# Optimization experiments

Measured on AMD Instinct MI355X. Metric: run time of the kernel, lower is better.

Reference implementation:

```python
import jax, jax.numpy as jnp
from jax import lax
import numpy as np

CASCADES = 3
CH = 16  # hidden channels of BasicBlock denoiser

# ---- finite-difference operators (equivalent to the sparse matrices) ----
# D has rows i<n-1: (-1 at i, +1 at i+1); last row zero.  (D v)[i] = v[i+1]-v[i], last = 0.

def fdiff(v, axis):
    d = jnp.diff(v, axis=axis)
    pad = [(0, 0)] * v.ndim
    pad[axis] = (0, 1)
    return jnp.pad(d, pad)

# Exact transpose: (D^T u)[j] = u[j-1] - u[j], with u[-1]=0 and the -u term dropped at j=n-1.

def fdiff_t(u, axis):
    n = u.shape[axis]
    pad_f = [(0, 0)] * u.ndim
    pad_f[axis] = (1, 0)
    u_prev = lax.slice_in_dim(jnp.pad(u, pad_f), 0, n, axis=axis)
    pad_b = [(0, 0)] * u.ndim
    pad_b[axis] = (0, 1)
    u_m = jnp.pad(lax.slice_in_dim(u, 0, n - 1, axis=axis), pad_b)
    return u_prev - u_m

# ---- BasicBlock: residual 3-layer 3D CNN denoiser ----

def _conv3d(h, w, b):
    out = lax.conv_general_dilated(h, w, (1, 1, 1), 'SAME',
                                   dimension_numbers=('NCDHW', 'OIDHW', 'NCDHW'))
    return out + b[None, :, None, None, None]

def basic_block(x, w1, b1, w2, b2, w3, b3):
    # x: [B, D, H, W]
    h = x[:, None]  # [B,1,D,H,W]
    h = jax.nn.relu(_conv3d(h, w1, b1))
    h = jax.nn.relu(_conv3d(h, w2, b2))
    h = _conv3d(h, w3, b3)
    return x + h[:, 0]

# ---- BeijingGeometry surrogate: parallel-beam fidelity A^T(sino - A t), A = sum over depth ----

def ite(t, sino):
    depth = t.shape[1]
    res = sino - t.sum(axis=1)          # [B, H, W]
    return jnp.broadcast_to(res[:, None] / depth, t.shape)


def setup_inputs() -> dict:
    key = jax.random.key(0)
    ks = jax.random.split(key, 12)
    B, D, H, W = 1, 64, 128, 128
    return {
        'image': jax.random.normal(ks[0], (B, D, H, W), jnp.float32),
        'sino': jax.random.normal(ks[1], (B, H, W), jnp.float32),
        'ae_w1': 0.05 * jax.random.normal(ks[2], (4, CH, 1, 3, 3, 3), jnp.float32),
        'ae_b1': jnp.zeros((4, CH), jnp.float32),
        'ae_w2': 0.05 * jax.random.normal(ks[3], (4, CH, CH, 3, 3, 3), jnp.float32),
        'ae_b2': jnp.zeros((4, CH), jnp.float32),
        'ae_w3': 0.05 * jax.random.normal(ks[4], (4, 1, CH, 3, 3, 3), jnp.float32),
        'ae_b3': jnp.zeros((4, 1), jnp.float32),
        'ntx': 0.1 * jax.random.normal(ks[5], (CASCADES,), jnp.float32),
        'nty': 0.1 * jax.random.normal(ks[6], (CASCADES,), jnp.float32),
        'ntz': 0.1 * jax.random.normal(ks[7], (CASCADES,), jnp.float32),
        'nt': 0.1 * jax.random.normal(ks[8], (CASCADES,), jnp.float32),
    }


def reference(image, sino, ae_w1, ae_b1, ae_w2, ae_b2, ae_w3, ae_b3, ntx, nty, ntz, nt):
    # axes: 1 = z (depth), 2 = y, 3 = x
    ae = lambda i, x: basic_block(x, ae_w1[i], ae_b1[i], ae_w2[i], ae_b2[i], ae_w3[i], ae_b3[i])
    t = image
    p = q = s = jnp.zeros_like(image)
    outs = [image]
    for c in range(CASCADES):
        z = t + ite(t, sino)
        pnew = ae(0, fdiff(z, 3))
        qnew = ae(1, fdiff(z, 2))
        snew = ae(2, fdiff(z, 1))
        znew = ae(3, z)
        p = p + ntx[c] * (p - pnew)
        q = q + nty[c] * (q - qnew)
        s = s + ntz[c] * (s - snew)
        z_ = t + nt[c] * (t - znew)
        t = fdiff_t(p, 3) + fdiff_t(q, 2) + fdiff_t(s, 1) + z_
        outs.append(t)
    return jnp.stack(outs)  # [cascades+1, B, D, H, W]
```

## Files before the change

### kernel.cpp

```cpp
#include <hip/hip_runtime.h>
#include <cstddef>

#define DD 64
#define HH 128
#define WW 128
#define HWC (HH * WW)
#define NN (DD * HWC)

#define PD 66
#define PH 130
#define PW 130
#define PHW (PH * PW)
#define PN (PD * PHW)

typedef __attribute__((ext_vector_type(8))) _Float16 half8;
typedef __attribute__((ext_vector_type(2))) _Float16 h2;
typedef __attribute__((ext_vector_type(4))) float f32x4;
typedef __attribute__((ext_vector_type(2))) float f32x2;

__device__ __forceinline__ int pcidx(int d, int h, int w) {
    return (d + 1) * PHW + (h + 1) * PW + (w + 1);
}

__device__ __forceinline__ float fdot2f(h2 a, h2 b, float c) {
#if __has_builtin(__builtin_amdgcn_fdot2)
    return __builtin_amdgcn_fdot2(a, b, c, false);
#else
    return fmaf((float)a[0], (float)b[0], fmaf((float)a[1], (float)b[1], c));
#endif
}

__global__ __launch_bounds__(256) void pad_zero(float* __restrict__ zP,
                                                float* __restrict__ dxP,
                                                float* __restrict__ dyP,
                                                float* __restrict__ dzP,
                                                _Float16* __restrict__ h1,
                                                _Float16* __restrict__ h2b) {
    int idx = blockIdx.x * 256 + threadIdx.x;
    if (idx >= PN) return;
    int d = idx / PHW;
    int rem = idx - d * PHW;
    int h = rem / PW;
    int w = rem - h * PW;
    bool pad = (d == 0) | (d == PD - 1) | (h == 0) | (h == PH - 1) |
               (w == 0) | (w == PW - 1);
    if (!pad) return;
    zP[idx] = 0.f;
    dxP[idx] = 0.f;
    dyP[idx] = 0.f;
    dzP[idx] = 0.f;
    half8 z = {};
    *(half8*)(h1 + (size_t)idx * 16) = z;
    *(half8*)(h1 + (size_t)idx * 16 + 8) = z;
    *(half8*)(h2b + (size_t)idx * 16) = z;
    *(half8*)(h2b + (size_t)idx * 16 + 8) = z;
}

__global__ __launch_bounds__(256) void init_k(const float* __restrict__ img,
                                              float* __restrict__ t,
                                              float* __restrict__ out0,
                                              float* __restrict__ p,
                                              float* __restrict__ q,
                                              float* __restrict__ s) {
    int i = blockIdx.x * 256 + threadIdx.x;
    float v = img[i];
    t[i] = v;
    out0[i] = v;
    p[i] = 0.f;
    q[i] = 0.f;
    s[i] = 0.f;
}

__global__ __launch_bounds__(256) void colsum_k(const float* __restrict__ t,
                                                const float* __restrict__ sino,
                                                float* __restrict__ r) {
    int hw = blockIdx.x * 256 + threadIdx.x;
    float sum = 0.f;
#pragma unroll 8
    for (int d = 0; d < DD; ++d) sum += t[d * HWC + hw];
    r[hw] = (sino[hw] - sum) * (1.0f / DD);
}

__global__ __launch_bounds__(256) void zdiff_k(const float* __restrict__ t,
                                               const float* __restrict__ r,
                                               float* __restrict__ zP,
                                               float* __restrict__ dxP,
                                               float* __restrict__ dyP,
                                               float* __restrict__ dzP) {
    int i = blockIdx.x * 256 + threadIdx.x;
    int w = i & (WW - 1);
    int h = (i >> 7) & (HH - 1);
    int d = i >> 14;
    int hw = i & (HWC - 1);
    int pc = pcidx(d, h, w);
    float tv = t[i];
    float rv = r[hw];
    float zv = tv + rv;
    zP[pc] = zv;
    dxP[pc] = (w < WW - 1) ? (t[i + 1] + r[hw + 1]) - zv : 0.f;
    dyP[pc] = (h < HH - 1) ? (t[i + WW] + r[hw + WW]) - zv : 0.f;
    dzP[pc] = (d < DD - 1) ? (t[i + HWC] - tv) : 0.f;
}

__global__ __launch_bounds__(256) void prep_w1(const float* __restrict__ w1,
                                               float* __restrict__ wA) {
    int idx = blockIdx.x * 256 + threadIdx.x;
    if (idx >= 1728) return;
    int bi = idx / 432;
    int rem = idx - bi * 432;
    int tap = rem >> 4;
    int co = rem & 15;
    wA[idx] = w1[bi * 432 + co * 27 + tap];
}

__global__ __launch_bounds__(256) void prep_w2(const float* __restrict__ w2,
                                               _Float16* __restrict__ wB) {
    int idx = blockIdx.x * 256 + threadIdx.x;
    if (idx >= 3584) return;
    int bi = idx / 896;
    int rem = idx - bi * 896;
    int kc = rem >> 4;
    int co = rem & 15;
    int tap = kc >> 1;
    int ci0 = (kc & 1) * 8;
    half8 v;
#pragma unroll
    for (int j = 0; j < 8; ++j) {
        float f = (tap < 27) ? w2[bi * 6912 + (co * 16 + ci0 + j) * 27 + tap] : 0.f;
        v[j] = (_Float16)f;
    }
    *(half8*)(wB + (size_t)idx * 8) = v;
}

__global__ __launch_bounds__(256) void prep_w3(const float* __restrict__ w3,
                                               h2* __restrict__ wC) {
    int idx = blockIdx.x * 256 + threadIdx.x;
    if (idx >= 864) return;
    int bi = idx / 216;
    int rem = idx - bi * 216;
    int tap = rem >> 3;
    int j = rem & 7;
    h2 v;
    v[0] = (_Float16)w3[bi * 432 + (2 * j) * 27 + tap];
    v[1] = (_Float16)w3[bi * 432 + (2 * j + 1) * 27 + tap];
    wC[idx] = v;
}

__global__ __launch_bounds__(256) void conv1_k(const float* __restrict__ x,
                                               const float* __restrict__ wA,
                                               const float* __restrict__ bias,
                                               _Float16* __restrict__ out) {
    int i = blockIdx.x * 256 + threadIdx.x;
    int w0 = (i & 31) * 4;
    int h = (i >> 5) & (HH - 1);
    int d = i >> 12;
    int pc = pcidx(d, h, w0);

    float acc[4][16];
#pragma unroll
    for (int o = 0; o < 4; ++o)
#pragma unroll
        for (int co = 0; co < 16; ++co) acc[o][co] = bias[co];

#pragma unroll
    for (int kd = 0; kd < 3; ++kd)
#pragma unroll
        for (int kh = 0; kh < 3; ++kh) {
            const float* base = x + pc + (kd - 1) * PHW + (kh - 1) * PW;
            f32x4 u = *(const f32x4*)(base - 1);
            f32x2 v = *(const f32x2*)(base + 3);
            float c[6] = {u[0], u[1], u[2], u[3], v[0], v[1]};
#pragma unroll
            for (int kw = 0; kw < 3; ++kw) {
                const int tap = (kd * 3 + kh) * 3 + kw;
                const float* wt = wA + tap * 16;
#pragma unroll
                for (int o = 0; o < 4; ++o) {
                    float vv = c[o + kw];
#pragma unroll
                    for (int co = 0; co < 16; ++co)
                        acc[o][co] = fmaf(vv, wt[co], acc[o][co]);
                }
            }
        }

#pragma unroll
    for (int o = 0; o < 4; ++o) {
        half8 lo, hi;
#pragma unroll
        for (int co = 0; co < 8; ++co) {
            lo[co] = (_Float16)fmaxf(acc[o][co], 0.f);
            hi[co] = (_Float16)fmaxf(acc[o][co + 8], 0.f);
        }
        _Float16* po = out + (size_t)(pc + o) * 16;
        *(half8*)po = lo;
        *(half8*)(po + 8) = hi;
    }
}

__global__ __launch_bounds__(256) void conv2_mfma(const _Float16* __restrict__ x,
                                                  const _Float16* __restrict__ wB,
                                                  const float* __restrict__ bias,
                                                  _Float16* __restrict__ out) {
    const int tid = threadIdx.x;
    const int lane = tid & 63;
    const int wid = tid >> 6;
    const int m64 = blockIdx.x * 256 + wid * 64;
    const int w0 = m64 & (WW - 1);
    const int h0 = (m64 >> 7) & (HH - 1);
    const int d0 = m64 >> 14;
    const int pc64 = pcidx(d0, h0, w0);
    const int l15 = lane & 15;
    const int lg = lane >> 4;
    const int tapSel = lg >> 1;
    const int ci0 = (lg & 1) * 8;

    int offl[14];
#pragma unroll
    for (int t = 0; t < 14; ++t) {
        int tap = 2 * t + tapSel;
        if (tap > 26) tap = 26;
        int kd = tap / 9;
        int kh = (tap / 3) % 3;
        int kw = tap % 3;
        offl[t] = (kd - 1) * PHW + (kh - 1) * PW + (kw - 1);
    }

    f32x4 acc0 = {0.f, 0.f, 0.f, 0.f};
    f32x4 acc1 = acc0, acc2 = acc0, acc3 = acc0;
    const int arow = pc64 + l15;

#pragma unroll
    for (int t = 0; t < 14; ++t) {
        half8 b = *(const half8*)(wB + (size_t)((t * 4 + lg) * 16 + l15) * 8);
        int ab = (arow + offl[t]) * 16 + ci0;
        half8 a0 = *(const half8*)(x + ab);
        half8 a1 = *(const half8*)(x + ab + 16 * 16);
        half8 a2 = *(const half8*)(x + ab + 32 * 16);
        half8 a3 = *(const half8*)(x + ab + 48 * 16);
        acc0 = __builtin_amdgcn_mfma_f32_16x16x32_f16(a0, b, acc0, 0, 0, 0);
        acc1 = __builtin_amdgcn_mfma_f32_16x16x32_f16(a1, b, acc1, 0, 0, 0);
        acc2 = __builtin_amdgcn_mfma_f32_16x16x32_f16(a2, b, acc2, 0, 0, 0);
        acc3 = __builtin_amdgcn_mfma_f32_16x16x32_f16(a3, b, acc3, 0, 0, 0);
    }

    float bc = bias[l15];
#pragma unroll
    for (int r = 0; r < 4; ++r) {
        f32x4 a = (r == 0) ? acc0 : (r == 1) ? acc1 : (r == 2) ? acc2 : acc3;
#pragma unroll
        for (int reg = 0; reg < 4; ++reg) {
            int prow = pc64 + r * 16 + lg * 4 + reg;
            float v = fmaxf(a[reg] + bc, 0.f);
            out[(size_t)prow * 16 + l15] = (_Float16)v;
        }
    }
}

__global__ __launch_bounds__(256) void conv3_k(const _Float16* __restrict__ x,
                                               const h2* __restrict__ wC,
                                               const float* __restrict__ bias,
                                               const float* __restrict__ residP,
                                               float* __restrict__ out) {
    int i = blockIdx.x * 256 + threadIdx.x;
    int w = i & (WW - 1);
    int h = (i >> 7) & (HH - 1);
    int dq = i >> 14;
    int d0 = dq * 4;
    int pc = pcidx(d0, h, w);

    float accA[4] = {0.f, 0.f, 0.f, 0.f};
    float accB[4] = {0.f, 0.f, 0.f, 0.f};

#pragma unroll
    for (int kh = 0; kh < 3; ++kh)
#pragma unroll
        for (int kw = 0; kw < 3; ++kw) {
            const _Float16* base =
                x + (size_t)(pc - PHW + (kh - 1) * PW + (kw - 1)) * 16;
#pragma unroll
            for (int p = 0; p < 6; ++p) {
                const _Float16* px = base + (size_t)p * PHW * 16;
                half8 v0 = *(const half8*)px;
                half8 v1 = *(const half8*)(px + 8);
#pragma unroll
                for (int kd = 0; kd < 3; ++kd) {
                    const int o = p - kd;
                    if (o < 0 || o > 3) continue;
                    const h2* wv = wC + (size_t)(kd * 9 + kh * 3 + kw) * 8;
                    h2 t2;
                    float a = accA[o], b = accB[o];
                    t2[0] = v0[0]; t2[1] = v0[1]; a = fdot2f(t2, wv[0], a);
                    t2[0] = v0[2]; t2[1] = v0[3]; b = fdot2f(t2, wv[1], b);
                    t2[0] = v0[4]; t2[1] = v0[5]; a = fdot2f(t2, wv[2], a);
                    t2[0] = v0[6]; t2[1] = v0[7]; b = fdot2f(t2, wv[3], b);
                    t2[0] = v1[0]; t2[1] = v1[1]; a = fdot2f(t2, wv[4], a);
                    t2[0] = v1[2]; t2[1] = v1[3]; b = fdot2f(t2, wv[5], b);
                    t2[0] = v1[4]; t2[1] = v1[5]; a = fdot2f(t2, wv[6], a);
                    t2[0] = v1[6]; t2[1] = v1[7]; b = fdot2f(t2, wv[7], b);
                    accA[o] = a; accB[o] = b;
                }
            }
        }

    float bc = bias[0];
    int ob = (d0 << 14) + (h << 7) + w;
#pragma unroll
    for (int o = 0; o < 4; ++o)
        out[ob + o * HWC] = residP[pc + o * PHW] + bc + (accA[o] + accB[o]);
}

__global__ __launch_bounds__(256) void update_k(const float* __restrict__ p0,
                                                const float* __restrict__ q0,
                                                const float* __restrict__ s0,
                                                const float* __restrict__ pn,
                                                const float* __restrict__ qn,
                                                const float* __restrict__ sn,
                                                const float* __restrict__ zn,
                                                float* __restrict__ t,
                                                float* __restrict__ p1,
                                                float* __restrict__ q1,
                                                float* __restrict__ s1,
                                                float* __restrict__ out,
                                                const float* __restrict__ ntx,
                                                const float* __restrict__ nty,
                                                const float* __restrict__ ntz,
                                                const float* __restrict__ nt,
                                                int c) {
    int i = blockIdx.x * 256 + threadIdx.x;
    int w = i & (WW - 1);
    int h = (i >> 7) & (HH - 1);
    int d = i >> 14;
    float cx = ntx[c], cy = nty[c], cz = ntz[c], ct = nt[c];

    float pu = p0[i] + cx * (p0[i] - pn[i]);
    float qu = q0[i] + cy * (q0[i] - qn[i]);
    float su = s0[i] + cz * (s0[i] - sn[i]);
    p1[i] = pu;
    q1[i] = qu;
    s1[i] = su;

    float tv = t[i];
    float zl = tv + ct * (tv - zn[i]);

    float acc = zl;
    if (w > 0) {
        float a = p0[i - 1];
        acc += a + cx * (a - pn[i - 1]);
    }
    if (w < WW - 1) acc -= pu;
    if (h > 0) {
        float a = q0[i - WW];
        acc += a + cy * (a - qn[i - WW]);
    }
    if (h < HH - 1) acc -= qu;
    if (d > 0) {
        float a = s0[i - HWC];
        acc += a + cz * (a - sn[i - HWC]);
    }
    if (d < DD - 1) acc -= su;

    t[i] = acc;
    out[i] = acc;
}

extern "C" void kernel_launch(void* const* d_in, const int* in_sizes, int n_in,
                              void* d_out, int out_size, void* d_ws, size_t ws_size,
                              hipStream_t stream) {
    const float* image = (const float*)d_in[0];
    const float* sino  = (const float*)d_in[1];
    const float* w1    = (const float*)d_in[2];
    const float* b1    = (const float*)d_in[3];
    const float* w2    = (const float*)d_in[4];
    const float* b2    = (const float*)d_in[5];
    const float* w3    = (const float*)d_in[6];
    const float* b3    = (const float*)d_in[7];
    const float* ntx   = (const float*)d_in[8];
    const float* nty   = (const float*)d_in[9];
    const float* ntz   = (const float*)d_in[10];
    const float* nt    = (const float*)d_in[11];

    float* out = (float*)d_out;
    float* ws  = (float*)d_ws;

    float* t     = ws;
    float* pbuf[2] = {ws + (size_t)1 * NN, ws + (size_t)4 * NN};
    float* qbuf[2] = {ws + (size_t)2 * NN, ws + (size_t)5 * NN};
    float* sbuf[2] = {ws + (size_t)3 * NN, ws + (size_t)6 * NN};
    float* pn = ws + (size_t)7 * NN;
    float* qn = ws + (size_t)8 * NN;
    float* sn = ws + (size_t)9 * NN;
    float* zn = ws + (size_t)10 * NN;
    float* r  = ws + (size_t)11 * NN;

    float* padbase = ws + (size_t)12 * NN;
    float* zP  = padbase;
    float* dxP = padbase + (size_t)1 * PN;
    float* dyP = padbase + (size_t)2 * PN;
    float* dzP = padbase + (size_t)3 * PN;
    _Float16* h1 = (_Float16*)(padbase + (size_t)4 * PN);
    _Float16* h2b = (_Float16*)(padbase + (size_t)12 * PN);
    _Float16* wBp = (_Float16*)(padbase + (size_t)20 * PN);
    h2* wCp = (h2*)(wBp + 4 * 7168);
    float* wAp = padbase + (size_t)20 * PN + 16384;

    const int NB = NN / 256;
    const int HB = HWC / 256;
    const int QB = NN / 4 / 256;
    const int PB = (PN + 255) / 256;

    pad_zero<<<PB, 256, 0, stream>>>(zP, dxP, dyP, dzP, h1, h2b);
    prep_w1<<<7, 256, 0, stream>>>(w1, wAp);
    prep_w2<<<14, 256, 0, stream>>>(w2, wBp);
    prep_w3<<<4, 256, 0, stream>>>(w3, wCp);
    init_k<<<NB, 256, 0, stream>>>(image, t, out, pbuf[0], qbuf[0], sbuf[0]);

    int cur = 0;
    for (int c = 0; c < 3; ++c) {
        colsum_k<<<HB, 256, 0, stream>>>(t, sino, r);
        zdiff_k<<<NB, 256, 0, stream>>>(t, r, zP, dxP, dyP, dzP);

        const float* xinP[4] = {dxP, dyP, dzP, zP};
        float*       oae[4]  = {pn, qn, sn, zn};
        for (int bi = 0; bi < 4; ++bi) {
            conv1_k<<<QB, 256, 0, stream>>>(xinP[bi], wAp + (size_t)bi * 432,
                                            b1 + (size_t)bi * 16, h1);
            conv2_mfma<<<NB, 256, 0, stream>>>(h1, wBp + (size_t)bi * 7168,
                                               b2 + (size_t)bi * 16, h2b);
            conv3_k<<<QB, 256, 0, stream>>>(h2b, wCp + (size_t)bi * 216,
                                            b3 + (size_t)bi, xinP[bi], oae[bi]);
        }

        update_k<<<NB, 256, 0, stream>>>(pbuf[cur], qbuf[cur], sbuf[cur],
                                         pn, qn, sn, zn, t,
                                         pbuf[1 - cur], qbuf[1 - cur], sbuf[1 - cur],
                                         out + (size_t)(c + 1) * NN,
                                         ntx, nty, ntz, nt, c);
        cur ^= 1;
    }
}
```

Measured before the change: 1.229 ms.

## Batch the four denoiser branches into single grid launches per conv stage

The four BasicBlock branches each ran their own conv1/conv2/conv3 launches. They now run as one launch per conv stage, using blockIdx.y to pick the branch, with a separate fp16 intermediate buffer per branch when the workspace is large enough. The three weight-prep kernels are also merged into one launch. This cuts the kernel launch count and the serialization between small grids, and fills the GPU better. In exchange it needs about four times the intermediate buffer memory and keeps a fallback path that loops over branches.

```diff
diff --git a/kernel.cpp b/kernel.cpp
--- a/kernel.cpp
+++ b/kernel.cpp
@@ -34,8 +34,9 @@
                                                 float* __restrict__ dxP,
                                                 float* __restrict__ dyP,
                                                 float* __restrict__ dzP,
-                                                _Float16* __restrict__ h1,
-                                                _Float16* __restrict__ h2b) {
+                                                _Float16* __restrict__ h1all,
+                                                _Float16* __restrict__ h2all,
+                                                int nb, size_t hstride) {
     int idx = blockIdx.x * 256 + threadIdx.x;
     if (idx >= PN) return;
     int d = idx / PHW;
@@ -50,10 +51,14 @@
     dyP[idx] = 0.f;
     dzP[idx] = 0.f;
     half8 z = {};
-    *(half8*)(h1 + (size_t)idx * 16) = z;
-    *(half8*)(h1 + (size_t)idx * 16 + 8) = z;
-    *(half8*)(h2b + (size_t)idx * 16) = z;
-    *(half8*)(h2b + (size_t)idx * 16 + 8) = z;
+    for (int k = 0; k < nb; ++k) {
+        _Float16* p1 = h1all + (size_t)k * hstride + (size_t)idx * 16;
+        _Float16* p2 = h2all + (size_t)k * hstride + (size_t)idx * 16;
+        *(half8*)p1 = z;
+        *(half8*)(p1 + 8) = z;
+        *(half8*)p2 = z;
+        *(half8*)(p2 + 8) = z;
+    }
 }
 
 __global__ __launch_bounds__(256) void init_k(const float* __restrict__ img,
@@ -102,54 +107,59 @@
     dzP[pc] = (d < DD - 1) ? (t[i + HWC] - tv) : 0.f;
 }
 
-__global__ __launch_bounds__(256) void prep_w1(const float* __restrict__ w1,
-                                               float* __restrict__ wA) {
+__global__ __launch_bounds__(256) void prep_all(const float* __restrict__ w1,
+                                                const float* __restrict__ w2,
+                                                const float* __restrict__ w3,
+                                                float* __restrict__ wA,
+                                                _Float16* __restrict__ wB,
+                                                h2* __restrict__ wC) {
     int idx = blockIdx.x * 256 + threadIdx.x;
-    if (idx >= 1728) return;
-    int bi = idx / 432;
-    int rem = idx - bi * 432;
-    int tap = rem >> 4;
-    int co = rem & 15;
-    wA[idx] = w1[bi * 432 + co * 27 + tap];
-}
-
-__global__ __launch_bounds__(256) void prep_w2(const float* __restrict__ w2,
-                                               _Float16* __restrict__ wB) {
-    int idx = blockIdx.x * 256 + threadIdx.x;
-    if (idx >= 3584) return;
-    int bi = idx / 896;
-    int rem = idx - bi * 896;
-    int kc = rem >> 4;
-    int co = rem & 15;
-    int tap = kc >> 1;
-    int ci0 = (kc & 1) * 8;
-    half8 v;
-#pragma unroll
-    for (int j = 0; j < 8; ++j) {
-        float f = (tap < 27) ? w2[bi * 6912 + (co * 16 + ci0 + j) * 27 + tap] : 0.f;
-        v[j] = (_Float16)f;
-    }
-    *(half8*)(wB + (size_t)idx * 8) = v;
-}
-
-__global__ __launch_bounds__(256) void prep_w3(const float* __restrict__ w3,
-                                               h2* __restrict__ wC) {
-    int idx = blockIdx.x * 256 + threadIdx.x;
-    if (idx >= 864) return;
-    int bi = idx / 216;
-    int rem = idx - bi * 216;
-    int tap = rem >> 3;
-    int j = rem & 7;
-    h2 v;
-    v[0] = (_Float16)w3[bi * 432 + (2 * j) * 27 + tap];
-    v[1] = (_Float16)w3[bi * 432 + (2 * j + 1) * 27 + tap];
-    wC[idx] = v;
-}
-
-__global__ __launch_bounds__(256) void conv1_k(const float* __restrict__ x,
+    if (idx < 1728) {
+        int bi = idx / 432;
+        int rem = idx - bi * 432;
+        int tap = rem >> 4;
+        int co = rem & 15;
+        wA[idx] = w1[bi * 432 + co * 27 + tap];
+    } else if (idx < 5312) {
+        int k = idx - 1728;
+        int bi = k / 896;
+        int rem = k - bi * 896;
+        int kc = rem >> 4;
+        int co = rem & 15;
+        int tap = kc >> 1;
+        int ci0 = (kc & 1) * 8;
+        half8 v;
+#pragma unroll
+        for (int j = 0; j < 8; ++j) {
+            float f = (tap < 27) ? w2[bi * 6912 + (co * 16 + ci0 + j) * 27 + tap]
+                                 : 0.f;
+            v[j] = (_Float16)f;
+        }
+        *(half8*)(wB + (size_t)k * 8) = v;
+    } else if (idx < 6176) {
+        int k = idx - 5312;
+        int bi = k / 216;
+        int rem = k - bi * 216;
+        int tap = rem >> 3;
+        int j = rem & 7;
+        h2 v;
+        v[0] = (_Float16)w3[bi * 432 + (2 * j) * 27 + tap];
+        v[1] = (_Float16)w3[bi * 432 + (2 * j + 1) * 27 + tap];
+        wC[k] = v;
+    }
+}
+
+__global__ __launch_bounds__(256) void conv1_b(const float* __restrict__ padbase,
                                                const float* __restrict__ wA,
-                                               const float* __restrict__ bias,
-                                               _Float16* __restrict__ out) {
+                                               const float* __restrict__ b1,
+                                               _Float16* __restrict__ h1all,
+                                               size_t hstride, int bi_base) {
+    const int bi = bi_base + blockIdx.y;
+    const float* x = padbase + (size_t)PN * ((bi + 1) & 3);
+    const float* wAb = wA + bi * 432;
+    const float* bias = b1 + bi * 16;
+    _Float16* out = h1all + (size_t)bi * hstride;
+
     int i = blockIdx.x * 256 + threadIdx.x;
     int w0 = (i & 31) * 4;
     int h = (i >> 5) & (HH - 1);
@@ -173,7 +183,7 @@
 #pragma unroll
             for (int kw = 0; kw < 3; ++kw) {
                 const int tap = (kd * 3 + kh) * 3 + kw;
-                const float* wt = wA + tap * 16;
+                const float* wt = wAb + tap * 16;
 #pragma unroll
                 for (int o = 0; o < 4; ++o) {
                     float vv = c[o + kw];
@@ -198,10 +208,17 @@
     }
 }
 
-__global__ __launch_bounds__(256) void conv2_mfma(const _Float16* __restrict__ x,
-                                                  const _Float16* __restrict__ wB,
-                                                  const float* __restrict__ bias,
-                                                  _Float16* __restrict__ out) {
+__global__ __launch_bounds__(256) void conv2_b(const _Float16* __restrict__ h1all,
+                                               const _Float16* __restrict__ wB,
+                                               const float* __restrict__ b2,
+                                               _Float16* __restrict__ h2all,
+                                               size_t hstride, int bi_base) {
+    const int bi = bi_base + blockIdx.y;
+    const _Float16* x = h1all + (size_t)bi * hstride;
+    const _Float16* wBb = wB + (size_t)bi * 7168;
+    const float* bias = b2 + bi * 16;
+    _Float16* out = h2all + (size_t)bi * hstride;
+
     const int tid = threadIdx.x;
     const int lane = tid & 63;
     const int wid = tid >> 6;
@@ -232,7 +249,7 @@
 
 #pragma unroll
     for (int t = 0; t < 14; ++t) {
-        half8 b = *(const half8*)(wB + (size_t)((t * 4 + lg) * 16 + l15) * 8);
+        half8 b = *(const half8*)(wBb + (size_t)((t * 4 + lg) * 16 + l15) * 8);
         int ab = (arow + offl[t]) * 16 + ci0;
         half8 a0 = *(const half8*)(x + ab);
         half8 a1 = *(const half8*)(x + ab + 16 * 16);
@@ -257,11 +274,19 @@
     }
 }
 
-__global__ __launch_bounds__(256) void conv3_k(const _Float16* __restrict__ x,
+__global__ __launch_bounds__(256) void conv3_b(const _Float16* __restrict__ h2all,
                                                const h2* __restrict__ wC,
-                                               const float* __restrict__ bias,
-                                               const float* __restrict__ residP,
-                                               float* __restrict__ out) {
+                                               const float* __restrict__ b3,
+                                               const float* __restrict__ padbase,
+                                               float* __restrict__ pnBase,
+                                               size_t hstride, int bi_base) {
+    const int bi = bi_base + blockIdx.y;
+    const _Float16* x = h2all + (size_t)bi * hstride;
+    const h2* wCb = wC + (size_t)bi * 216;
+    const float* residP = padbase + (size_t)PN * ((bi + 1) & 3);
+    float* out = pnBase + (size_t)bi * NN;
+    const float bc = b3[bi];
+
     int i = blockIdx.x * 256 + threadIdx.x;
     int w = i & (WW - 1);
     int h = (i >> 7) & (HH - 1);
@@ -287,7 +312,7 @@
                 for (int kd = 0; kd < 3; ++kd) {
                     const int o = p - kd;
                     if (o < 0 || o > 3) continue;
-                    const h2* wv = wC + (size_t)(kd * 9 + kh * 3 + kw) * 8;
+                    const h2* wv = wCb + (size_t)(kd * 9 + kh * 3 + kw) * 8;
                     h2 t2;
                     float a = accA[o], b = accB[o];
                     t2[0] = v0[0]; t2[1] = v0[1]; a = fdot2f(t2, wv[0], a);
@@ -303,7 +328,6 @@
             }
         }
 
-    float bc = bias[0];
     int ob = (d0 << 14) + (h << 7) + w;
 #pragma unroll
     for (int o = 0; o < 4; ++o)
@@ -388,9 +412,6 @@
     float* qbuf[2] = {ws + (size_t)2 * NN, ws + (size_t)5 * NN};
     float* sbuf[2] = {ws + (size_t)3 * NN, ws + (size_t)6 * NN};
     float* pn = ws + (size_t)7 * NN;
-    float* qn = ws + (size_t)8 * NN;
-    float* sn = ws + (size_t)9 * NN;
-    float* zn = ws + (size_t)10 * NN;
     float* r  = ws + (size_t)11 * NN;
 
     float* padbase = ws + (size_t)12 * NN;
@@ -398,21 +419,28 @@
     float* dxP = padbase + (size_t)1 * PN;
     float* dyP = padbase + (size_t)2 * PN;
     float* dzP = padbase + (size_t)3 * PN;
-    _Float16* h1 = (_Float16*)(padbase + (size_t)4 * PN);
-    _Float16* h2b = (_Float16*)(padbase + (size_t)12 * PN);
-    _Float16* wBp = (_Float16*)(padbase + (size_t)20 * PN);
+
+    const size_t HS = (size_t)PN * 16;
+    _Float16* h1all = (_Float16*)(padbase + (size_t)4 * PN);
+    size_t needed_batched =
+        ((size_t)12 * NN + (size_t)4 * PN + 17000) * 4 + 2 * 4 * HS * 2;
+    bool batched = ws_size >= needed_batched;
+    int nb = batched ? 4 : 1;
+    size_t hstride = batched ? HS : 0;
+
+    _Float16* h2all = h1all + (size_t)nb * HS;
+    float* wtail = (float*)(h2all + (size_t)nb * HS);
+    _Float16* wBp = (_Float16*)wtail;
     h2* wCp = (h2*)(wBp + 4 * 7168);
-    float* wAp = padbase + (size_t)20 * PN + 16384;
+    float* wAp = (float*)(wCp + 4 * 216);
 
     const int NB = NN / 256;
     const int HB = HWC / 256;
     const int QB = NN / 4 / 256;
     const int PB = (PN + 255) / 256;
 
-    pad_zero<<<PB, 256, 0, stream>>>(zP, dxP, dyP, dzP, h1, h2b);
-    prep_w1<<<7, 256, 0, stream>>>(w1, wAp);
-    prep_w2<<<14, 256, 0, stream>>>(w2, wBp);
-    prep_w3<<<4, 256, 0, stream>>>(w3, wCp);
+    pad_zero<<<PB, 256, 0, stream>>>(zP, dxP, dyP, dzP, h1all, h2all, nb, HS);
+    prep_all<<<25, 256, 0, stream>>>(w1, w2, w3, wAp, wBp, wCp);
     init_k<<<NB, 256, 0, stream>>>(image, t, out, pbuf[0], qbuf[0], sbuf[0]);
 
     int cur = 0;
@@ -420,19 +448,27 @@
         colsum_k<<<HB, 256, 0, stream>>>(t, sino, r);
         zdiff_k<<<NB, 256, 0, stream>>>(t, r, zP, dxP, dyP, dzP);
 
-        const float* xinP[4] = {dxP, dyP, dzP, zP};
-        float*       oae[4]  = {pn, qn, sn, zn};
-        for (int bi = 0; bi < 4; ++bi) {
-            conv1_k<<<QB, 256, 0, stream>>>(xinP[bi], wAp + (size_t)bi * 432,
-                                            b1 + (size_t)bi * 16, h1);
-            conv2_mfma<<<NB, 256, 0, stream>>>(h1, wBp + (size_t)bi * 7168,
-                                               b2 + (size_t)bi * 16, h2b);
-            conv3_k<<<QB, 256, 0, stream>>>(h2b, wCp + (size_t)bi * 216,
-                                            b3 + (size_t)bi, xinP[bi], oae[bi]);
+        if (batched) {
+            conv1_b<<<dim3(QB, 4), 256, 0, stream>>>(padbase, wAp, b1, h1all,
+                                                     hstride, 0);
+            conv2_b<<<dim3(NB, 4), 256, 0, stream>>>(h1all, wBp, b2, h2all,
+                                                     hstride, 0);
+            conv3_b<<<dim3(QB, 4), 256, 0, stream>>>(h2all, wCp, b3, padbase,
+                                                     pn, hstride, 0);
+        } else {
+            for (int bi = 0; bi < 4; ++bi) {
+                conv1_b<<<dim3(QB, 1), 256, 0, stream>>>(padbase, wAp, b1,
+                                                         h1all, 0, bi);
+                conv2_b<<<dim3(NB, 1), 256, 0, stream>>>(h1all, wBp, b2,
+                                                         h2all, 0, bi);
+                conv3_b<<<dim3(QB, 1), 256, 0, stream>>>(h2all, wCp, b3,
+                                                         padbase, pn, 0, bi);
+            }
         }
 
         update_k<<<NB, 256, 0, stream>>>(pbuf[cur], qbuf[cur], sbuf[cur],
-                                         pn, qn, sn, zn, t,
+                                         pn, pn + NN, pn + 2 * (size_t)NN,
+                                         pn + 3 * (size_t)NN, t,
                                          pbuf[1 - cur], qbuf[1 - cur], sbuf[1 - cur],
                                          out + (size_t)(c + 1) * NN,
                                          ntx, nty, ntz, nt, c);
```

New measurement: 1.223 ms. About the same (-0.4%).

## Stage conv2 input halo tile in LDS via direct global-to-LDS loads

Applied to the files above, without the earlier changes.

The middle 16->16 channel convolution now stages the padded input tile, 2 rows by 4 planes in the halo region with 130-wide rows, into shared memory using global_load_lds. A swizzled half-row layout is used to reduce bank conflicts. MFMA A-operands are then read from LDS instead of issuing 27-tap redundant global loads, which cuts L2/global traffic. Each block now covers two h-rows of 128 instead of four 64-voxel strips. The three weight-prep kernels are merged into one launch, and the buffer layout is compacted. The LDS footprint of about 53KB per block may reduce occupancy.

```diff
diff --git a/kernel.cpp b/kernel.cpp
--- a/kernel.cpp
+++ b/kernel.cpp
@@ -102,48 +102,46 @@
     dzP[pc] = (d < DD - 1) ? (t[i + HWC] - tv) : 0.f;
 }
 
-__global__ __launch_bounds__(256) void prep_w1(const float* __restrict__ w1,
-                                               float* __restrict__ wA) {
+__global__ __launch_bounds__(256) void prep_all(const float* __restrict__ w1,
+                                                const float* __restrict__ w2,
+                                                const float* __restrict__ w3,
+                                                float* __restrict__ wA,
+                                                _Float16* __restrict__ wB,
+                                                h2* __restrict__ wC) {
     int idx = blockIdx.x * 256 + threadIdx.x;
-    if (idx >= 1728) return;
-    int bi = idx / 432;
-    int rem = idx - bi * 432;
-    int tap = rem >> 4;
-    int co = rem & 15;
-    wA[idx] = w1[bi * 432 + co * 27 + tap];
-}
-
-__global__ __launch_bounds__(256) void prep_w2(const float* __restrict__ w2,
-                                               _Float16* __restrict__ wB) {
-    int idx = blockIdx.x * 256 + threadIdx.x;
-    if (idx >= 3584) return;
-    int bi = idx / 896;
-    int rem = idx - bi * 896;
-    int kc = rem >> 4;
-    int co = rem & 15;
-    int tap = kc >> 1;
-    int ci0 = (kc & 1) * 8;
-    half8 v;
-#pragma unroll
-    for (int j = 0; j < 8; ++j) {
-        float f = (tap < 27) ? w2[bi * 6912 + (co * 16 + ci0 + j) * 27 + tap] : 0.f;
-        v[j] = (_Float16)f;
-    }
-    *(half8*)(wB + (size_t)idx * 8) = v;
-}
-
-__global__ __launch_bounds__(256) void prep_w3(const float* __restrict__ w3,
-                                               h2* __restrict__ wC) {
-    int idx = blockIdx.x * 256 + threadIdx.x;
-    if (idx >= 864) return;
-    int bi = idx / 216;
-    int rem = idx - bi * 216;
-    int tap = rem >> 3;
-    int j = rem & 7;
-    h2 v;
-    v[0] = (_Float16)w3[bi * 432 + (2 * j) * 27 + tap];
-    v[1] = (_Float16)w3[bi * 432 + (2 * j + 1) * 27 + tap];
-    wC[idx] = v;
+    if (idx < 1728) {
+        int bi = idx / 432;
+        int rem = idx - bi * 432;
+        int tap = rem >> 4;
+        int co = rem & 15;
+        wA[idx] = w1[bi * 432 + co * 27 + tap];
+    } else if (idx < 5312) {
+        int k = idx - 1728;
+        int bi = k / 896;
+        int rem = k - bi * 896;
+        int kc = rem >> 4;
+        int co = rem & 15;
+        int tap = kc >> 1;
+        int ci0 = (kc & 1) * 8;
+        half8 v;
+#pragma unroll
+        for (int j = 0; j < 8; ++j) {
+            float f = (tap < 27) ? w2[bi * 6912 + (co * 16 + ci0 + j) * 27 + tap]
+                                 : 0.f;
+            v[j] = (_Float16)f;
+        }
+        *(half8*)(wB + (size_t)k * 8) = v;
+    } else if (idx < 6176) {
+        int k = idx - 5312;
+        int bi = k / 216;
+        int rem = k - bi * 216;
+        int tap = rem >> 3;
+        int j = rem & 7;
+        h2 v;
+        v[0] = (_Float16)w3[bi * 432 + (2 * j) * 27 + tap];
+        v[1] = (_Float16)w3[bi * 432 + (2 * j + 1) * 27 + tap];
+        wC[k] = v;
+    }
 }
 
 __global__ __launch_bounds__(256) void conv1_k(const float* __restrict__ x,
@@ -198,24 +196,43 @@
     }
 }
 
-__global__ __launch_bounds__(256) void conv2_mfma(const _Float16* __restrict__ x,
-                                                  const _Float16* __restrict__ wB,
-                                                  const float* __restrict__ bias,
-                                                  _Float16* __restrict__ out) {
+__global__ __launch_bounds__(256) void conv2_lds(const _Float16* __restrict__ x,
+                                                 const _Float16* __restrict__ wB,
+                                                 const float* __restrict__ bias,
+                                                 _Float16* __restrict__ out) {
+    __shared__ __align__(16) _Float16 lds[3328 * 8];
+
     const int tid = threadIdx.x;
     const int lane = tid & 63;
     const int wid = tid >> 6;
-    const int m64 = blockIdx.x * 256 + wid * 64;
-    const int w0 = m64 & (WW - 1);
-    const int h0 = (m64 >> 7) & (HH - 1);
-    const int d0 = m64 >> 14;
-    const int pc64 = pcidx(d0, h0, w0);
+    const int m256 = blockIdx.x * 256;
+    const int h0 = (m256 >> 7) & (HH - 1);
+    const int d0 = m256 >> 14;
+    const int origin = d0 * PHW + h0 * PW;
+
+    for (int it = 0; it < 13; ++it) {
+        int P = it * 256 + tid;
+        int G = P ^ ((P >> 3) & 1);
+        int lin = G >> 1;
+        int hf = G & 1;
+        unsigned seg = (unsigned)lin / 130u;
+        int wx = lin - (int)seg * 130;
+        int dz = (int)seg >> 2, hy = (int)seg & 3;
+        const _Float16* src =
+            x + ((size_t)(origin + dz * PHW + hy * PW + wx) * 16 + hf * 8);
+        _Float16* dst = lds + ((size_t)(it * 256 + wid * 64) * 8);
+        __builtin_amdgcn_global_load_lds(
+            (const __attribute__((address_space(1))) void*)src,
+            (__attribute__((address_space(3))) void*)dst, 16, 0, 0);
+    }
+    __syncthreads();
+
     const int l15 = lane & 15;
     const int lg = lane >> 4;
     const int tapSel = lg >> 1;
-    const int ci0 = (lg & 1) * 8;
-
-    int offl[14];
+    const int hf0 = lg & 1;
+
+    int rowt[14];
 #pragma unroll
     for (int t = 0; t < 14; ++t) {
         int tap = 2 * t + tapSel;
@@ -223,27 +240,29 @@
         int kd = tap / 9;
         int kh = (tap / 3) % 3;
         int kw = tap % 3;
-        offl[t] = (kd - 1) * PHW + (kh - 1) * PW + (kw - 1);
+        rowt[t] = (kd * 4 + (wid >> 1) + kh) * 130 + (wid & 1) * 64 + l15 + kw;
     }
 
     f32x4 acc0 = {0.f, 0.f, 0.f, 0.f};
     f32x4 acc1 = acc0, acc2 = acc0, acc3 = acc0;
-    const int arow = pc64 + l15;
 
 #pragma unroll
     for (int t = 0; t < 14; ++t) {
         half8 b = *(const half8*)(wB + (size_t)((t * 4 + lg) * 16 + l15) * 8);
-        int ab = (arow + offl[t]) * 16 + ci0;
-        half8 a0 = *(const half8*)(x + ab);
-        half8 a1 = *(const half8*)(x + ab + 16 * 16);
-        half8 a2 = *(const half8*)(x + ab + 32 * 16);
-        half8 a3 = *(const half8*)(x + ab + 48 * 16);
+        int r = rowt[t];
+        int g = r * 2 + (hf0 ^ ((r >> 2) & 1));
+        const _Float16* pa = lds + (size_t)g * 8;
+        half8 a0 = *(const half8*)(pa);
+        half8 a1 = *(const half8*)(pa + 32 * 8);
+        half8 a2 = *(const half8*)(pa + 64 * 8);
+        half8 a3 = *(const half8*)(pa + 96 * 8);
         acc0 = __builtin_amdgcn_mfma_f32_16x16x32_f16(a0, b, acc0, 0, 0, 0);
         acc1 = __builtin_amdgcn_mfma_f32_16x16x32_f16(a1, b, acc1, 0, 0, 0);
         acc2 = __builtin_amdgcn_mfma_f32_16x16x32_f16(a2, b, acc2, 0, 0, 0);
         acc3 = __builtin_amdgcn_mfma_f32_16x16x32_f16(a3, b, acc3, 0, 0, 0);
     }
 
+    const int pc64 = pcidx(d0, h0 + (wid >> 1), (wid & 1) * 64);
     float bc = bias[l15];
 #pragma unroll
     for (int r = 0; r < 4; ++r) {
@@ -388,9 +407,6 @@
     float* qbuf[2] = {ws + (size_t)2 * NN, ws + (size_t)5 * NN};
     float* sbuf[2] = {ws + (size_t)3 * NN, ws + (size_t)6 * NN};
     float* pn = ws + (size_t)7 * NN;
-    float* qn = ws + (size_t)8 * NN;
-    float* sn = ws + (size_t)9 * NN;
-    float* zn = ws + (size_t)10 * NN;
     float* r  = ws + (size_t)11 * NN;
 
     float* padbase = ws + (size_t)12 * NN;
@@ -398,11 +414,13 @@
     float* dxP = padbase + (size_t)1 * PN;
     float* dyP = padbase + (size_t)2 * PN;
     float* dzP = padbase + (size_t)3 * PN;
-    _Float16* h1 = (_Float16*)(padbase + (size_t)4 * PN);
-    _Float16* h2b = (_Float16*)(padbase + (size_t)12 * PN);
-    _Float16* wBp = (_Float16*)(padbase + (size_t)20 * PN);
+
+    const size_t HS = (size_t)PN * 16;
+    _Float16* h1  = (_Float16*)(padbase + (size_t)4 * PN);
+    _Float16* h2b = h1 + HS;
+    _Float16* wBp = h2b + HS;
     h2* wCp = (h2*)(wBp + 4 * 7168);
-    float* wAp = padbase + (size_t)20 * PN + 16384;
+    float* wAp = (float*)(wCp + 4 * 216);
 
     const int NB = NN / 256;
     const int HB = HWC / 256;
@@ -410,9 +428,7 @@
     const int PB = (PN + 255) / 256;
 
     pad_zero<<<PB, 256, 0, stream>>>(zP, dxP, dyP, dzP, h1, h2b);
-    prep_w1<<<7, 256, 0, stream>>>(w1, wAp);
-    prep_w2<<<14, 256, 0, stream>>>(w2, wBp);
-    prep_w3<<<4, 256, 0, stream>>>(w3, wCp);
+    prep_all<<<25, 256, 0, stream>>>(w1, w2, w3, wAp, wBp, wCp);
     init_k<<<NB, 256, 0, stream>>>(image, t, out, pbuf[0], qbuf[0], sbuf[0]);
 
     int cur = 0;
@@ -421,18 +437,19 @@
         zdiff_k<<<NB, 256, 0, stream>>>(t, r, zP, dxP, dyP, dzP);
 
         const float* xinP[4] = {dxP, dyP, dzP, zP};
-        float*       oae[4]  = {pn, qn, sn, zn};
         for (int bi = 0; bi < 4; ++bi) {
             conv1_k<<<QB, 256, 0, stream>>>(xinP[bi], wAp + (size_t)bi * 432,
                                             b1 + (size_t)bi * 16, h1);
-            conv2_mfma<<<NB, 256, 0, stream>>>(h1, wBp + (size_t)bi * 7168,
-                                               b2 + (size_t)bi * 16, h2b);
+            conv2_lds<<<NB, 256, 0, stream>>>(h1, wBp + (size_t)bi * 7168,
+                                              b2 + (size_t)bi * 16, h2b);
             conv3_k<<<QB, 256, 0, stream>>>(h2b, wCp + (size_t)bi * 216,
-                                            b3 + (size_t)bi, xinP[bi], oae[bi]);
+                                            b3 + (size_t)bi, xinP[bi],
+                                            pn + (size_t)bi * NN);
         }
 
         update_k<<<NB, 256, 0, stream>>>(pbuf[cur], qbuf[cur], sbuf[cur],
-                                         pn, qn, sn, zn, t,
+                                         pn, pn + NN, pn + 2 * (size_t)NN,
+                                         pn + 3 * (size_t)NN, t,
                                          pbuf[1 - cur], qbuf[1 - cur], sbuf[1 - cur],
                                          out + (size_t)(c + 1) * NN,
                                          ntx, nty, ntz, nt, c);
```

Result: faster. 1.069 ms (-13.0%).
